# Kernel optimization log

Hardware: AMD Instinct MI355X
Metric: run time of the kernel (lower is better)

## Reference

```python
import jax, jax.numpy as jnp
import numpy as np

P = 16          # patch size (patch_height == patch_width)
DIM = 768       # feature dim
K = 9           # number of anchor boxes (arange(0, 9) in source)
# anchor_boxes = [(h_ratio, w_ratio) for h in (2,4,8) for w in (2,4,8)]
BOX_H = jnp.array([2., 2., 2., 4., 4., 4., 8., 8., 8.], dtype=jnp.float32)
BOX_W = jnp.array([2., 4., 8., 2., 4., 8., 2., 4., 8.], dtype=jnp.float32)


def setup_inputs() -> dict:
    key = jax.random.key(0)
    k0, k1, k2, k3 = jax.random.split(key, 4)
    b, c, h, w = 32, 3, 512, 512
    img = jax.random.normal(k0, (b, c, h, w), dtype=jnp.float32)
    # patch-embed stand-in for feature_extraction_ViT: (c*P*P) -> DIM
    w_patch = jax.random.normal(k1, (c * P * P, DIM), dtype=jnp.float32) * 0.02
    w_reg = jax.random.normal(k2, (DIM, 4 * K), dtype=jnp.float32) * 0.02
    b_reg = jnp.zeros((4 * K,), dtype=jnp.float32)
    w_obj = jax.random.normal(k3, (DIM, K), dtype=jnp.float32) * 0.02
    b_obj = jnp.zeros((K,), dtype=jnp.float32)
    return {"img": img, "w_patch": w_patch, "w_reg": w_reg, "b_reg": b_reg,
            "w_obj": w_obj, "b_obj": b_obj}


def reference(img, w_patch, w_reg, b_reg, w_obj, b_obj):
    b, c, h, w = img.shape
    fh, fw = h // P, w // P
    # --- feature_extraction_ViT (patch embedding) -> feature map [b, fh, fw, DIM]
    patches = img.reshape(b, c, fh, P, fw, P).transpose(0, 2, 4, 1, 3, 5)
    patches = patches.reshape(b, fh, fw, c * P * P)
    feat = patches @ w_patch                                  # [b, fh, fw, DIM]
    # --- RPN: regs [b, fh, fw, K, 4], objectness [b, fh, fw, K, 1]
    regs = (feat @ w_reg + b_reg).reshape(b, fh, fw, K, 4)    # separate_anchor_boxes, s=4
    is_object = jax.nn.sigmoid(feat @ w_obj + b_obj)[..., None]
    # --- anchor-box coordinate decoding (memory-bound broadcast pipeline)
    wgrid = jnp.arange(0, w, P, dtype=jnp.float32)            # step = patch_width
    hgrid = jnp.arange(0, h, P, dtype=jnp.float32)            # step = patch_height
    width_coords = wgrid[None, None, :, None, None] + regs[..., 0:1]
    height_coords = hgrid[None, :, None, None, None] + regs[..., 1:2]
    width_abs = width_coords + BOX_W[None, None, None, :, None] * regs[..., 2:3]
    height_abs = height_coords + BOX_H[None, None, None, :, None] * regs[..., 3:4]
    batch_idx = jnp.broadcast_to(
        jnp.arange(b, dtype=jnp.float32)[:, None, None, None, None], (b, fh, fw, K, 1))
    k_idx = jnp.broadcast_to(
        jnp.arange(K, dtype=jnp.float32)[None, None, None, :, None], (b, fh, fw, K, 1))
    merged = jnp.concatenate(
        [width_coords, height_coords, width_abs, height_abs, batch_idx, is_object, k_idx],
        axis=-1)                                              # [b, fh, fw, K, 7]
    tensor_reshaped = merged.reshape(-1, 7)                   # (b h w k) x
    return tensor_reshaped
```

## Files before the change

kernel.cpp:

```cpp
#include <hip/hip_runtime.h>

typedef __attribute__((ext_vector_type(8))) short bf16x8;
typedef __attribute__((ext_vector_type(4))) float f32x4;

__device__ __forceinline__ unsigned short f2bf(float f) {
    unsigned int u = __float_as_uint(f);
    u = (u + 0x7FFFu + ((u >> 16) & 1u)) >> 16;
    return (unsigned short)u;
}

__global__ __launch_bounds__(256) void wcomb_partial(
        const float* __restrict__ wp, const float* __restrict__ wreg,
        const float* __restrict__ wobj, float* __restrict__ part) {
    __shared__ float Al[64][132];
    __shared__ float Bl[48][132];
    const int t  = threadIdx.x;
    const int d0 = blockIdx.x * 128;
    const int k0 = blockIdx.y * 64;

    #pragma unroll
    for (int i = 0; i < 8; ++i) {
        int e = i * 256 + t;
        int row = e >> 5, dq = e & 31;
        *(f32x4*)&Al[row][dq * 4] =
            *(const f32x4*)&wp[(size_t)(k0 + row) * 768 + d0 + dq * 4];
    }
    #pragma unroll
    for (int i = 0; i < 24; ++i) {
        int e = i * 256 + t;
        int d = e / 48, n = e - d * 48;
        float v = 0.f;
        if (n < 36)      v = wreg[(size_t)(d0 + d) * 36 + n];
        else if (n < 45) v = wobj[(size_t)(d0 + d) * 9 + (n - 36)];
        Bl[n][d] = v;
    }
    __syncthreads();

    const int r0 = (t & 15) * 4;
    const int n0 = (t >> 4) * 3;
    float acc[4][3] = {};
    for (int ds = 0; ds < 32; ++ds) {
        f32x4 a[4], bv[3];
        #pragma unroll
        for (int i = 0; i < 4; ++i) a[i] = *(const f32x4*)&Al[r0 + i][ds * 4];
        #pragma unroll
        for (int j = 0; j < 3; ++j) bv[j] = *(const f32x4*)&Bl[n0 + j][ds * 4];
        #pragma unroll
        for (int i = 0; i < 4; ++i)
            #pragma unroll
            for (int j = 0; j < 3; ++j)
                acc[i][j] += a[i].x * bv[j].x + a[i].y * bv[j].y
                           + a[i].z * bv[j].z + a[i].w * bv[j].w;
    }
    #pragma unroll
    for (int i = 0; i < 4; ++i)
        #pragma unroll
        for (int j = 0; j < 3; ++j)
            part[((size_t)blockIdx.x * 768 + k0 + r0 + i) * 48 + n0 + j] = acc[i][j];
}

__global__ __launch_bounds__(256) void wcomb_reduce(
        const float* __restrict__ part, unsigned short* __restrict__ wct) {
    const int k = blockIdx.x * 256 + threadIdx.x;
    const int n = blockIdx.y;
    float s = 0.f;
    if (n < 45) {
        #pragma unroll
        for (int dc = 0; dc < 6; ++dc) s += part[((size_t)dc * 768 + k) * 48 + n];
    }
    wct[(size_t)n * 768 + k] = f2bf(s);
}

__global__ __launch_bounds__(256) void detector_main(
        const float* __restrict__ img, const unsigned short* __restrict__ wct,
        const float* __restrict__ breg, const float* __restrict__ bobj,
        float* __restrict__ out) {
    __shared__ float Co[64][49];

    const int t    = threadIdx.x;
    const int lane = t & 63;
    const int wid  = t >> 6;
    const int cl   = lane & 15;
    const int q    = lane >> 4;
    const int wg   = blockIdx.x * 4 + wid;
    const int fj0  = (wg & 1) * 16;
    const int fi   = (wg >> 1) & 31;
    const int b    = wg >> 6;

    const float* ap = img + (size_t)b * 786432
        + (size_t)(fi * 16 + (q >> 1)) * 512 + (fj0 + cl) * 16 + (q & 1) * 8;
    const unsigned short* bp = wct + cl * 768 + q * 8;

    f32x4 acc0 = {0.f,0.f,0.f,0.f}, acc1 = acc0, acc2 = acc0;

    f32x4 ca0 = *(const f32x4*)ap;
    f32x4 ca1 = *(const f32x4*)(ap + 4);
    bf16x8 cb0 = *(const bf16x8*)(bp);
    bf16x8 cb1 = *(const bf16x8*)(bp + 12288);
    bf16x8 cb2 = *(const bf16x8*)(bp + 24576);

    #pragma unroll 4
    for (int kk = 0; kk < 24; ++kk) {
        const int astep = ((kk & 7) == 7) ? 254976 : 1024;
        const float* nap = (kk == 23) ? ap : ap + astep;
        const unsigned short* nbp = (kk == 23) ? bp : bp + 32;
        f32x4 na0 = *(const f32x4*)nap;
        f32x4 na1 = *(const f32x4*)(nap + 4);
        bf16x8 nb0 = *(const bf16x8*)(nbp);
        bf16x8 nb1 = *(const bf16x8*)(nbp + 12288);
        bf16x8 nb2 = *(const bf16x8*)(nbp + 24576);

        bf16x8 af;
        af[0] = (short)f2bf(ca0.x); af[1] = (short)f2bf(ca0.y);
        af[2] = (short)f2bf(ca0.z); af[3] = (short)f2bf(ca0.w);
        af[4] = (short)f2bf(ca1.x); af[5] = (short)f2bf(ca1.y);
        af[6] = (short)f2bf(ca1.z); af[7] = (short)f2bf(ca1.w);
        acc0 = __builtin_amdgcn_mfma_f32_16x16x32_bf16(af, cb0, acc0, 0, 0, 0);
        acc1 = __builtin_amdgcn_mfma_f32_16x16x32_bf16(af, cb1, acc1, 0, 0, 0);
        acc2 = __builtin_amdgcn_mfma_f32_16x16x32_bf16(af, cb2, acc2, 0, 0, 0);

        ap = nap; bp = nbp;
        ca0 = na0; ca1 = na1; cb0 = nb0; cb1 = nb1; cb2 = nb2;
    }

    #pragma unroll
    for (int r = 0; r < 4; ++r) {
        Co[wid * 16 + q * 4 + r][ 0 + cl] = acc0[r];
        Co[wid * 16 + q * 4 + r][16 + cl] = acc1[r];
        Co[wid * 16 + q * 4 + r][32 + cl] = acc2[r];
    }
    __syncthreads();

    for (int rr = lane; rr < 144; rr += 64) {
        int cell = rr / 9, k = rr - cell * 9;
        int fj = fj0 + cell;
        float v0 = Co[wid * 16 + cell][4 * k + 0] + breg[4 * k + 0];
        float v1 = Co[wid * 16 + cell][4 * k + 1] + breg[4 * k + 1];
        float v2 = Co[wid * 16 + cell][4 * k + 2] + breg[4 * k + 2];
        float v3 = Co[wid * 16 + cell][4 * k + 3] + breg[4 * k + 3];
        float lg = Co[wid * 16 + cell][36 + k] + bobj[k];
        float obj = 1.f / (1.f + __expf(-lg));
        float wc = (float)(fj * 16) + v0;
        float hc = (float)(fi * 16) + v1;
        float wa = wc + (float)(2 << (k % 3)) * v2;
        float ha = hc + (float)(2 << (k / 3)) * v3;
        float* o = out + (size_t)(((b * 32 + fi) * 32 + fj) * 9 + k) * 7;
        o[0] = wc; o[1] = hc; o[2] = wa; o[3] = ha;
        o[4] = (float)b; o[5] = obj; o[6] = (float)k;
    }
}

extern "C" void kernel_launch(void* const* d_in, const int* in_sizes, int n_in,
                              void* d_out, int out_size, void* d_ws, size_t ws_size,
                              hipStream_t stream) {
    const float* img  = (const float*)d_in[0];
    const float* wp   = (const float*)d_in[1];
    const float* wreg = (const float*)d_in[2];
    const float* breg = (const float*)d_in[3];
    const float* wobj = (const float*)d_in[4];
    const float* bobj = (const float*)d_in[5];
    float* out = (float*)d_out;

    float* part = (float*)d_ws;
    unsigned short* wct = (unsigned short*)((char*)d_ws + 6 * 768 * 48 * 4);

    wcomb_partial<<<dim3(6, 12), 256, 0, stream>>>(wp, wreg, wobj, part);
    wcomb_reduce<<<dim3(3, 48), 256, 0, stream>>>(part, wct);
    detector_main<<<512, 256, 0, stream>>>(img, wct, breg, bobj, out);
}
```

Baseline: 189.2 us.

## Fuse weight-combine kernels and split detector K-loop across wave pairs

The two-stage weight combination (partial GEMM plus reduce) becomes one kernel in which each block loops over all six D-chunks and writes bf16 output directly. This removes a launch and the partial-sum workspace round trip. The detector kernel now splits the 768-long reduction between two waves per tile and sums their halves in shared memory, doubling the grid to 1024 blocks to raise parallelism and memory-level concurrency. The trade-off is that the fused weight kernel has only 48 blocks with serial chunks, and the detector needs extra LDS reduction work.

New measurement: 277.0 us. 46.4% more time.

```diff
diff --git a/kernel.cpp b/kernel.cpp
--- a/kernel.cpp
+++ b/kernel.cpp
@@ -9,87 +9,72 @@
     return (unsigned short)u;
 }
 
-__global__ __launch_bounds__(256) void wcomb_partial(
+__global__ __launch_bounds__(256) void wcomb_fused(
         const float* __restrict__ wp, const float* __restrict__ wreg,
-        const float* __restrict__ wobj, float* __restrict__ part) {
-    __shared__ float Al[64][132];
+        const float* __restrict__ wobj, unsigned short* __restrict__ wct) {
+    __shared__ float Al[16][132];
     __shared__ float Bl[48][132];
     const int t  = threadIdx.x;
-    const int d0 = blockIdx.x * 128;
-    const int k0 = blockIdx.y * 64;
+    const int kb = blockIdx.x * 16;
+    const int k  = t >> 4;
+    const int n0 = (t & 15) * 3;
 
-    #pragma unroll
-    for (int i = 0; i < 8; ++i) {
-        int e = i * 256 + t;
-        int row = e >> 5, dq = e & 31;
-        *(f32x4*)&Al[row][dq * 4] =
-            *(const f32x4*)&wp[(size_t)(k0 + row) * 768 + d0 + dq * 4];
+    float acc[3] = {0.f, 0.f, 0.f};
+    for (int dc = 0; dc < 6; ++dc) {
+        const int d0 = dc * 128;
+        #pragma unroll
+        for (int i = 0; i < 2; ++i) {
+            int e = i * 256 + t;
+            int row = e >> 5, v = e & 31;
+            *(f32x4*)&Al[row][v * 4] =
+                *(const f32x4*)&wp[(size_t)(kb + row) * 768 + d0 + v * 4];
+        }
+        #pragma unroll
+        for (int i = 0; i < 24; ++i) {
+            int e = i * 256 + t;
+            int d = e / 48, n = e - d * 48;
+            float v = 0.f;
+            if (n < 36)      v = wreg[(size_t)(d0 + d) * 36 + n];
+            else if (n < 45) v = wobj[(size_t)(d0 + d) * 9 + (n - 36)];
+            Bl[n][d] = v;
+        }
+        __syncthreads();
+        #pragma unroll 8
+        for (int ds = 0; ds < 32; ++ds) {
+            f32x4 a = *(const f32x4*)&Al[k][ds * 4];
+            #pragma unroll
+            for (int j = 0; j < 3; ++j) {
+                f32x4 b = *(const f32x4*)&Bl[n0 + j][ds * 4];
+                acc[j] += a.x * b.x + a.y * b.y + a.z * b.z + a.w * b.w;
+            }
+        }
+        __syncthreads();
     }
     #pragma unroll
-    for (int i = 0; i < 24; ++i) {
-        int e = i * 256 + t;
-        int d = e / 48, n = e - d * 48;
-        float v = 0.f;
-        if (n < 36)      v = wreg[(size_t)(d0 + d) * 36 + n];
-        else if (n < 45) v = wobj[(size_t)(d0 + d) * 9 + (n - 36)];
-        Bl[n][d] = v;
-    }
-    __syncthreads();
-
-    const int r0 = (t & 15) * 4;
-    const int n0 = (t >> 4) * 3;
-    float acc[4][3] = {};
-    for (int ds = 0; ds < 32; ++ds) {
-        f32x4 a[4], bv[3];
-        #pragma unroll
-        for (int i = 0; i < 4; ++i) a[i] = *(const f32x4*)&Al[r0 + i][ds * 4];
-        #pragma unroll
-        for (int j = 0; j < 3; ++j) bv[j] = *(const f32x4*)&Bl[n0 + j][ds * 4];
-        #pragma unroll
-        for (int i = 0; i < 4; ++i)
-            #pragma unroll
-            for (int j = 0; j < 3; ++j)
-                acc[i][j] += a[i].x * bv[j].x + a[i].y * bv[j].y
-                           + a[i].z * bv[j].z + a[i].w * bv[j].w;
-    }
-    #pragma unroll
-    for (int i = 0; i < 4; ++i)
-        #pragma unroll
-        for (int j = 0; j < 3; ++j)
-            part[((size_t)blockIdx.x * 768 + k0 + r0 + i) * 48 + n0 + j] = acc[i][j];
-}
-
-__global__ __launch_bounds__(256) void wcomb_reduce(
-        const float* __restrict__ part, unsigned short* __restrict__ wct) {
-    const int k = blockIdx.x * 256 + threadIdx.x;
-    const int n = blockIdx.y;
-    float s = 0.f;
-    if (n < 45) {
-        #pragma unroll
-        for (int dc = 0; dc < 6; ++dc) s += part[((size_t)dc * 768 + k) * 48 + n];
-    }
-    wct[(size_t)n * 768 + k] = f2bf(s);
+    for (int j = 0; j < 3; ++j)
+        wct[(size_t)(n0 + j) * 768 + kb + k] = f2bf(acc[j]);
 }
 
 __global__ __launch_bounds__(256) void detector_main(
         const float* __restrict__ img, const unsigned short* __restrict__ wct,
         const float* __restrict__ breg, const float* __restrict__ bobj,
         float* __restrict__ out) {
-    __shared__ float Co[64][49];
+    __shared__ float Co[4][16][49];
 
     const int t    = threadIdx.x;
     const int lane = t & 63;
     const int wid  = t >> 6;
     const int cl   = lane & 15;
     const int q    = lane >> 4;
-    const int wg   = blockIdx.x * 4 + wid;
-    const int fj0  = (wg & 1) * 16;
-    const int fi   = (wg >> 1) & 31;
-    const int b    = wg >> 6;
+    const int kh   = wid & 1;
+    const int tg   = blockIdx.x * 2 + (wid >> 1);
+    const int fj0  = (tg & 1) * 16;
+    const int fi   = (tg >> 1) & 31;
+    const int b    = tg >> 6;
 
-    const float* ap = img + (size_t)b * 786432
+    const float* ap = img + (size_t)b * 786432 + (size_t)kh * 266240
         + (size_t)(fi * 16 + (q >> 1)) * 512 + (fj0 + cl) * 16 + (q & 1) * 8;
-    const unsigned short* bp = wct + cl * 768 + q * 8;
+    const unsigned short* bp = wct + cl * 768 + q * 8 + kh * 384;
 
     f32x4 acc0 = {0.f,0.f,0.f,0.f}, acc1 = acc0, acc2 = acc0;
 
@@ -100,10 +85,11 @@
     bf16x8 cb2 = *(const bf16x8*)(bp + 24576);
 
     #pragma unroll 4
-    for (int kk = 0; kk < 24; ++kk) {
+    for (int i = 0; i < 12; ++i) {
+        const int kk = kh * 12 + i;
         const int astep = ((kk & 7) == 7) ? 254976 : 1024;
-        const float* nap = (kk == 23) ? ap : ap + astep;
-        const unsigned short* nbp = (kk == 23) ? bp : bp + 32;
+        const float* nap = (i == 11) ? ap : ap + astep;
+        const unsigned short* nbp = (i == 11) ? bp : bp + 32;
         f32x4 na0 = *(const f32x4*)nap;
         f32x4 na1 = *(const f32x4*)(nap + 4);
         bf16x8 nb0 = *(const bf16x8*)(nbp);
@@ -125,28 +111,33 @@
 
     #pragma unroll
     for (int r = 0; r < 4; ++r) {
-        Co[wid * 16 + q * 4 + r][ 0 + cl] = acc0[r];
-        Co[wid * 16 + q * 4 + r][16 + cl] = acc1[r];
-        Co[wid * 16 + q * 4 + r][32 + cl] = acc2[r];
+        Co[wid][q * 4 + r][ 0 + cl] = acc0[r];
+        Co[wid][q * 4 + r][16 + cl] = acc1[r];
+        Co[wid][q * 4 + r][32 + cl] = acc2[r];
     }
     __syncthreads();
 
-    for (int rr = lane; rr < 144; rr += 64) {
-        int cell = rr / 9, k = rr - cell * 9;
-        int fj = fj0 + cell;
-        float v0 = Co[wid * 16 + cell][4 * k + 0] + breg[4 * k + 0];
-        float v1 = Co[wid * 16 + cell][4 * k + 1] + breg[4 * k + 1];
-        float v2 = Co[wid * 16 + cell][4 * k + 2] + breg[4 * k + 2];
-        float v3 = Co[wid * 16 + cell][4 * k + 3] + breg[4 * k + 3];
-        float lg = Co[wid * 16 + cell][36 + k] + bobj[k];
+    for (int rr = t; rr < 288; rr += 256) {
+        int tp   = rr / 144;
+        int rw   = rr - tp * 144;
+        int cell = rw / 9, k = rw - cell * 9;
+        int tgd  = blockIdx.x * 2 + tp;
+        int dfj  = (tgd & 1) * 16 + cell;
+        int dfi  = (tgd >> 1) & 31;
+        int db   = tgd >> 6;
+        float v0 = Co[2*tp][cell][4*k+0] + Co[2*tp+1][cell][4*k+0] + breg[4*k+0];
+        float v1 = Co[2*tp][cell][4*k+1] + Co[2*tp+1][cell][4*k+1] + breg[4*k+1];
+        float v2 = Co[2*tp][cell][4*k+2] + Co[2*tp+1][cell][4*k+2] + breg[4*k+2];
+        float v3 = Co[2*tp][cell][4*k+3] + Co[2*tp+1][cell][4*k+3] + breg[4*k+3];
+        float lg = Co[2*tp][cell][36+k]  + Co[2*tp+1][cell][36+k]  + bobj[k];
         float obj = 1.f / (1.f + __expf(-lg));
-        float wc = (float)(fj * 16) + v0;
-        float hc = (float)(fi * 16) + v1;
+        float wc = (float)(dfj * 16) + v0;
+        float hc = (float)(dfi * 16) + v1;
         float wa = wc + (float)(2 << (k % 3)) * v2;
         float ha = hc + (float)(2 << (k / 3)) * v3;
-        float* o = out + (size_t)(((b * 32 + fi) * 32 + fj) * 9 + k) * 7;
+        float* o = out + (size_t)(((db * 32 + dfi) * 32 + dfj) * 9 + k) * 7;
         o[0] = wc; o[1] = hc; o[2] = wa; o[3] = ha;
-        o[4] = (float)b; o[5] = obj; o[6] = (float)k;
+        o[4] = (float)db; o[5] = obj; o[6] = (float)k;
     }
 }
 
@@ -161,10 +152,8 @@
     const float* bobj = (const float*)d_in[5];
     float* out = (float*)d_out;
 
-    float* part = (float*)d_ws;
-    unsigned short* wct = (unsigned short*)((char*)d_ws + 6 * 768 * 48 * 4);
+    unsigned short* wct = (unsigned short*)d_ws;
 
-    wcomb_partial<<<dim3(6, 12), 256, 0, stream>>>(wp, wreg, wobj, part);
-    wcomb_reduce<<<dim3(3, 48), 256, 0, stream>>>(part, wct);
-    detector_main<<<512, 256, 0, stream>>>(img, wct, breg, bobj, out);
+    wcomb_fused<<<48, 256, 0, stream>>>(wp, wreg, wobj, wct);
+    detector_main<<<1024, 256, 0, stream>>>(img, wct, breg, bobj, out);
 }
```
